# Optimization experiments

Measured on AMD Instinct MI355X. Metric: run time of the kernel, lower is better.

Reference implementation:

```python
import jax, jax.numpy as jnp
import numpy as np
import math

def setup_inputs() -> dict:
    key = jax.random.key(0)
    k1, k2, k3 = jax.random.split(key, 3)
    B, S, E = 2, 2048, 1024
    H, D = 16, 64
    inputs = jax.random.normal(k1, (B, S, E), dtype=jnp.float32)
    Wqkv = jax.random.uniform(k2, (E, 3 * H * D), minval=-0.1, maxval=0.1, dtype=jnp.float32)
    Wo = jax.random.uniform(k3, (H * D, E), minval=-0.1, maxval=0.1, dtype=jnp.float32)
    return {"inputs": inputs, "Wqkv": Wqkv, "Wo": Wo, "nhead": H}

def reference(inputs, Wqkv, Wo, nhead):
    B, S, E = inputs.shape
    H = int(nhead)
    D = Wqkv.shape[1] // (3 * H)
    causal, ghost = True, True

    qkv = jnp.matmul(inputs, Wqkv)                       # (B, S, 3*H*D)
    qkv = qkv.reshape(B, S, 3, H, D)
    Q = qkv[:, :, 0].transpose(0, 2, 1, 3)               # (B, H, S, D)
    K = qkv[:, :, 1].transpose(0, 2, 1, 3)
    V = qkv[:, :, 2].transpose(0, 2, 1, 3)

    scores = jnp.einsum('bhqd,bhkd->bhqk', Q, K) / math.sqrt(D)
    if causal:
        neg_inf = jnp.float32(-jnp.inf)
        mask = jnp.where(jnp.triu(jnp.ones((S, S), dtype=bool), k=1), neg_inf, jnp.float32(0.0))
        scores = scores + mask  # broadcast over (B, H)

    # ghost softmax: standard stable softmax but denominator gets +1
    z = jnp.exp(scores - jnp.max(scores, axis=-1, keepdims=True))
    denom = jnp.sum(z, axis=-1, keepdims=True)
    if ghost:
        denom = denom + jnp.float32(1.0)
    attn = z / denom                                      # (B, H, S, S)

    A = jnp.einsum('bhqk,bhkd->bhqd', attn, V)            # (B, H, S, D)
    A = A.transpose(0, 2, 1, 3).reshape(B, S, H * D)      # (B, S, H*D)
    return jnp.matmul(A, Wo)
```

## Files before the change

### kernel.cpp

```cpp
#include <hip/hip_runtime.h>

typedef float    f32x4  __attribute__((ext_vector_type(4)));
typedef _Float16 half8  __attribute__((ext_vector_type(8)));
typedef _Float16 half4v __attribute__((ext_vector_type(4)));

#define MFMA16(a,b,c) __builtin_amdgcn_mfma_f32_16x16x32_f16(a,b,c,0,0,0)

__device__ __forceinline__ float exp2_fast(float x){
  float y; asm("v_exp_f32 %0, %1" : "=v"(y) : "v"(x)); return y;
}
__device__ __forceinline__ void gload_lds16(const _Float16* g, _Float16* l){
  __builtin_amdgcn_global_load_lds(
      (const __attribute__((address_space(1))) unsigned int*)(g),
      (__attribute__((address_space(3))) unsigned int*)(l),
      16, 0, 0);
}

#define S_LEN 2048
#define E_DIM 1024
#define H_NUM 16
#define D_DIM 64
#define NBH   32
#define M_ROWS 4096
#define N3    3072
#define LOG2E 1.44269504089f

__global__ __launch_bounds__(256) void prep_kernel(
    const float* __restrict__ X, const float* __restrict__ Wqkv,
    const float* __restrict__ Wo,
    _Float16* __restrict__ Xh, _Float16* __restrict__ Wqh,
    _Float16* __restrict__ Woh)
{
  __shared__ float tile[32][33];
  const int blk = blockIdx.x, tid = threadIdx.x;
  if (blk < 4096){
    const int i = blk * 256 + tid;
    const float4 v = reinterpret_cast<const float4*>(X)[i];
    half4v h;
    h[0] = (_Float16)v.x; h[1] = (_Float16)v.y;
    h[2] = (_Float16)v.z; h[3] = (_Float16)v.w;
    *reinterpret_cast<half4v*>(&Xh[(size_t)i*4]) = h;
    return;
  }
  const float* in; _Float16* out; int R, C, bx, by;
  if (blk < 4096 + 3072){
    const int b2 = blk - 4096;
    in = Wqkv; out = Wqh; R = E_DIM; C = N3;
    bx = (b2 % 96) * 32; by = (b2 / 96) * 32;
  } else {
    const int b2 = blk - 7168;
    in = Wo; out = Woh; R = E_DIM; C = E_DIM;
    bx = (b2 % 32) * 32; by = (b2 / 32) * 32;
  }
  const int tx = tid & 31, ty = tid >> 5;
#pragma unroll
  for (int i = ty; i < 32; i += 8)
    tile[i][tx] = in[(size_t)(by + i) * C + bx + tx];
  __syncthreads();
#pragma unroll
  for (int i = ty; i < 32; i += 8)
    out[(size_t)(bx + i) * R + by + tx] = (_Float16)tile[tx][i];
}

template<int EPI>
__global__ __launch_bounds__(256, 3) void gemm97(
    const _Float16* __restrict__ A, const _Float16* __restrict__ B,
    int Kdim, int Ndim, float* __restrict__ Cout,
    _Float16* __restrict__ qh, _Float16* __restrict__ kh, _Float16* __restrict__ vh)
{
  __shared__ __align__(16) _Float16 sA[128][64], sB[128][64];
  const int tid = threadIdx.x;
  const int m0 = blockIdx.y * 128, n0 = blockIdx.x * 128;
  const int wid = tid >> 6, lane = tid & 63;
  const int wr = (wid >> 1) * 64, wc = (wid & 1) * 64;
  const int lr = lane & 15, lc = lane >> 4;
  const int ldrow = lane >> 3;
  const int ldcol = ((lane & 7) ^ ldrow) * 8;
  const int swz = (lr & 7) << 4;

  f32x4 acc[4][4] = {};
  const int nK = Kdim >> 6;
  for (int ks = 0; ks < nK; ++ks){
    const int k0 = ks << 6;
#pragma unroll
    for (int cc = 0; cc < 4; ++cc){
      const int c = wid * 4 + cc;
      const int row = c * 8 + ldrow;
      gload_lds16(&A[(size_t)(m0 + row) * Kdim + k0 + ldcol], &sA[c*8][0]);
      gload_lds16(&B[(size_t)(n0 + row) * Kdim + k0 + ldcol], &sB[c*8][0]);
    }
    __syncthreads();
    const char* ab = (const char*)&sA[0][0];
    const char* bb = (const char*)&sB[0][0];
#pragma unroll
    for (int kk = 0; kk < 64; kk += 32){
      half8 fa[4], fb[4];
#pragma unroll
      for (int t = 0; t < 4; ++t){
        fa[t] = *reinterpret_cast<const half8*>(
            ab + (wr + t*16 + lr)*128 + ((kk*2 + lc*16) ^ swz));
        fb[t] = *reinterpret_cast<const half8*>(
            bb + (wc + t*16 + lr)*128 + ((kk*2 + lc*16) ^ swz));
      }
#pragma unroll
      for (int mt = 0; mt < 4; ++mt)
#pragma unroll
        for (int nt = 0; nt < 4; ++nt)
          acc[mt][nt] = MFMA16(fa[mt], fb[nt], acc[mt][nt]);
    }
    __syncthreads();
  }
#pragma unroll
  for (int mt = 0; mt < 4; ++mt)
#pragma unroll
    for (int nt = 0; nt < 4; ++nt)
#pragma unroll
      for (int r = 0; r < 4; ++r){
        const int m = m0 + wr + mt*16 + lc*4 + r;
        const int n = n0 + wc + nt*16 + lr;
        float v = acc[mt][nt][r];
        if (EPI == 0){
          Cout[(size_t)m * Ndim + n] = v;
        } else {
          const int t = n >> 10, rem = n & 1023, hh = rem >> 6, d = rem & 63;
          const int b = m >> 11, s = m & 2047;
          const int bh = b * H_NUM + hh;
          if (t == 0) v *= (0.125f * LOG2E);
          size_t o;
          if (t == 2)  o = ((size_t)bh * D_DIM + d) * S_LEN + s;
          else         o = ((size_t)bh * S_LEN + s) * D_DIM + d;
          _Float16* ph = (t == 0) ? qh : (t == 1) ? kh : vh;
          ph[o] = (_Float16)v;
        }
      }
}

__global__ __launch_bounds__(256, 4) void gemm64(
    const _Float16* __restrict__ A, const _Float16* __restrict__ B,
    int Kdim, int Ndim, float* __restrict__ Cout)
{
  __shared__ __align__(16) _Float16 sA[64][64], sB[128][64];
  const int tid = threadIdx.x;
  const int m0 = blockIdx.y * 64, n0 = blockIdx.x * 128;
  const int wid = tid >> 6, lane = tid & 63;
  const int wr = (wid >> 1) * 32, wc = (wid & 1) * 64;
  const int lr = lane & 15, lc = lane >> 4;
  const int ldrow = lane >> 3;
  const int ldcol = ((lane & 7) ^ ldrow) * 8;
  const int swz = (lr & 7) << 4;

  f32x4 acc[2][4] = {};
  const int nK = Kdim >> 6;
  for (int ks = 0; ks < nK; ++ks){
    const int k0 = ks << 6;
#pragma unroll
    for (int cc = 0; cc < 2; ++cc){
      const int c = wid * 2 + cc;
      const int row = c * 8 + ldrow;
      gload_lds16(&A[(size_t)(m0 + row) * Kdim + k0 + ldcol], &sA[c*8][0]);
    }
#pragma unroll
    for (int cc = 0; cc < 4; ++cc){
      const int c = wid * 4 + cc;
      const int row = c * 8 + ldrow;
      gload_lds16(&B[(size_t)(n0 + row) * Kdim + k0 + ldcol], &sB[c*8][0]);
    }
    __syncthreads();
    const char* ab = (const char*)&sA[0][0];
    const char* bb = (const char*)&sB[0][0];
#pragma unroll
    for (int kk = 0; kk < 64; kk += 32){
      half8 fa[2], fb[4];
#pragma unroll
      for (int t = 0; t < 2; ++t)
        fa[t] = *reinterpret_cast<const half8*>(
            ab + (wr + t*16 + lr)*128 + ((kk*2 + lc*16) ^ swz));
#pragma unroll
      for (int t = 0; t < 4; ++t)
        fb[t] = *reinterpret_cast<const half8*>(
            bb + (wc + t*16 + lr)*128 + ((kk*2 + lc*16) ^ swz));
#pragma unroll
      for (int mt = 0; mt < 2; ++mt)
#pragma unroll
        for (int nt = 0; nt < 4; ++nt)
          acc[mt][nt] = MFMA16(fa[mt], fb[nt], acc[mt][nt]);
    }
    __syncthreads();
  }
#pragma unroll
  for (int mt = 0; mt < 2; ++mt)
#pragma unroll
    for (int nt = 0; nt < 4; ++nt)
#pragma unroll
      for (int r = 0; r < 4; ++r){
        const int m = m0 + wr + mt*16 + lc*4 + r;
        const int n = n0 + wc + nt*16 + lr;
        Cout[(size_t)m * Ndim + n] = acc[mt][nt][r];
      }
}

__global__ __launch_bounds__(256, 6) void attn_partial(
    const _Float16* __restrict__ Qh, const _Float16* __restrict__ Kh,
    const _Float16* __restrict__ Vth,
    _Float16* __restrict__ Opart, float* __restrict__ Spart)
{
  __shared__ __align__(16) _Float16 sK[64][64];
  __shared__ __align__(16) _Float16 sV[64][64];
  __shared__ __align__(16) _Float16 sP[4][16][64];
  const int tid = threadIdx.x, wid = tid >> 6, lane = tid & 63;
  const int id  = blockIdx.x;
  const int xcd = id & 7, seq = id >> 3;
  const int bh  = xcd + 8 * (seq & 3);
  const int rest = seq >> 2;
  const int qt  = 31 - (rest >> 1);
  const int half = rest & 1;
  const int h0 = (qt + 1) >> 1;
  const int t0 = half ? h0 : 0;
  const int t1 = half ? (qt + 1) : h0;
  const int q0 = qt * 64;
  const int lr = lane & 15, lc = lane >> 4;
  const int swz = (lr & 7) << 4;
  const size_t base = (size_t)bh * S_LEN * D_DIM;

  const int pidx = (bh * 32 + qt) * 2 + half;
  _Float16* Op = Opart + (size_t)pidx * 4096;
  float*    Sp = Spart + (size_t)pidx * 192;

  if (t1 <= t0){
#pragma unroll
    for (int dt = 0; dt < 4; ++dt)
#pragma unroll
      for (int r = 0; r < 4; ++r)
        Op[(wid*16 + lc*4 + r)*64 + dt*16 + lr] = (_Float16)0.f;
    if (lane < 16){
      Sp[wid*16 + lr] = -1e30f;
      Sp[64 + wid*16 + lr] = 0.f;
      Sp[128 + wid*16 + lr] = -1e30f;
    }
    return;
  }

  const int lrow = lane >> 3;
  const int cswz = ((lane & 7) ^ lrow) * 8;

  auto stage = [&](int t){
    const int kv0 = t * 64;
#pragma unroll
    for (int cc = 0; cc < 2; ++cc){
      const int c = wid * 2 + cc;
      const int row = c * 8 + lrow;
      gload_lds16(&Kh[base + (size_t)(kv0 + row) * D_DIM + cswz], &sK[c*8][0]);
      gload_lds16(&Vth[base + (size_t)row * S_LEN + kv0 + cswz], &sV[c*8][0]);
    }
  };

  half8 fq[2];
  {
    const int qrow = q0 + wid*16 + lr;
#pragma unroll
    for (int kc = 0; kc < 2; ++kc)
      fq[kc] = *reinterpret_cast<const half8*>(&Qh[base + (size_t)qrow * 64 + kc*32 + lc*8]);
  }

  f32x4 acc[4] = {};
  float m = -1e30f, l = 0.f, tm = -1e30f;

#pragma unroll 1
  for (int t = t0; t < t1; ++t){
    __syncthreads();
    stage(t);
    __syncthreads();

    const char* kb = (const char*)&sK[0][0];
    f32x4 sc[4];
    __builtin_amdgcn_s_setprio(1);
#pragma unroll
    for (int nt = 0; nt < 4; ++nt){
      f32x4 z = {};
#pragma unroll
      for (int kc = 0; kc < 2; ++kc){
        const half8 fk = *reinterpret_cast<const half8*>(
            kb + (nt*16 + lr)*128 + ((kc*64 + lc*16) ^ swz));
        z = MFMA16(fk, fq[kc], z);
      }
      sc[nt] = z;
    }
    __builtin_amdgcn_s_setprio(0);

    if (t == qt){
#pragma unroll
      for (int nt = 0; nt < 4; ++nt)
#pragma unroll
        for (int r = 0; r < 4; ++r)
          if (nt*16 + lc*4 + r > wid*16 + lr) sc[nt][r] = -1e30f;
    }

    f32x4 a;
#pragma unroll
    for (int j = 0; j < 4; ++j)
      a[j] = fmaxf(fmaxf(sc[0][j], sc[1][j]), fmaxf(sc[2][j], sc[3][j]));
    float mx = fmaxf(fmaxf(a[0], a[1]), fmaxf(a[2], a[3]));
    mx = fmaxf(mx, __shfl_xor(mx, 16));
    mx = fmaxf(mx, __shfl_xor(mx, 32));
    tm = fmaxf(tm, mx);

    if (__any(mx > m + 8.0f)){
      const float mn = fmaxf(m, mx);
      const float s = exp2_fast(m - mn);
      l *= s; m = mn;
      float rs[4];
#pragma unroll
      for (int r = 0; r < 4; ++r)
        rs[r] = __shfl(s, (lc << 4) | (lc*4 + r), 64);
#pragma unroll
      for (int dt = 0; dt < 4; ++dt)
#pragma unroll
        for (int r = 0; r < 4; ++r) acc[dt][r] *= rs[r];
    }

    f32x4 ssum = {};
#pragma unroll
    for (int nt = 0; nt < 4; ++nt){
#pragma unroll
      for (int r = 0; r < 4; ++r) sc[nt][r] = exp2_fast(sc[nt][r] - m);
      ssum += sc[nt];
    }
    float s1 = (ssum[0] + ssum[1]) + (ssum[2] + ssum[3]);
    s1 += __shfl_xor(s1, 16);
    s1 += __shfl_xor(s1, 32);
    l += s1;

    char* pw = (char*)&sP[wid][0][0];
#pragma unroll
    for (int nt = 0; nt < 4; ++nt){
      int2 pk;
      pk.x = __builtin_bit_cast(int, __builtin_amdgcn_cvt_pkrtz(sc[nt][0], sc[nt][1]));
      pk.y = __builtin_bit_cast(int, __builtin_amdgcn_cvt_pkrtz(sc[nt][2], sc[nt][3]));
      *reinterpret_cast<int2*>(pw + lr*128 + ((nt*32 + lc*8) ^ swz)) = pk;
    }

    const half8 pa0 = *reinterpret_cast<const half8*>(pw + lr*128 + ((lc*16) ^ swz));
    const half8 pa1 = *reinterpret_cast<const half8*>(pw + lr*128 + ((64 + lc*16) ^ swz));

    const char* vb = (const char*)&sV[0][0];
    __builtin_amdgcn_s_setprio(1);
#pragma unroll
    for (int dt = 0; dt < 4; ++dt){
#pragma unroll
      for (int kc = 0; kc < 2; ++kc){
        const half8 fv = *reinterpret_cast<const half8*>(
            vb + (dt*16 + lr)*128 + ((kc*64 + lc*16) ^ swz));
        acc[dt] = MFMA16(kc ? pa1 : pa0, fv, acc[dt]);
      }
    }
    __builtin_amdgcn_s_setprio(0);
  }

#pragma unroll
  for (int dt = 0; dt < 4; ++dt)
#pragma unroll
    for (int r = 0; r < 4; ++r)
      Op[(wid*16 + lc*4 + r)*64 + dt*16 + lr] = (_Float16)acc[dt][r];
  if (lane < 16){
    Sp[wid*16 + lr] = m;
    Sp[64 + wid*16 + lr] = l;
    Sp[128 + wid*16 + lr] = tm;
  }
}

__global__ __launch_bounds__(256) void attn_merge(
    const _Float16* __restrict__ Opart, const float* __restrict__ Spart,
    _Float16* __restrict__ Ao)
{
  const int id = blockIdx.x;
  const int bh = id >> 5, qt = id & 31;
  const int tid = threadIdx.x;
  const int row = tid >> 2, seg = tid & 3;
  const int p0 = (bh * 32 + qt) * 2, p1 = p0 + 1;
  const float* S1 = Spart + (size_t)p0 * 192;
  const float* S2 = Spart + (size_t)p1 * 192;
  const float m1 = S1[row], l1 = S1[64 + row], t1 = S1[128 + row];
  const float m2 = S2[row], l2 = S2[64 + row], t2 = S2[128 + row];
  const float M  = fmaxf(m1, m2);
  const float w1 = exp2_fast(m1 - M), w2 = exp2_fast(m2 - M);
  const float den = l1 * w1 + l2 * w2 + exp2_fast(fmaxf(t1, t2) - M);
  const float inv = 1.0f / den;
  const half8* O1 = reinterpret_cast<const half8*>(Opart + (size_t)p0 * 4096 + row * 64 + seg * 16);
  const half8* O2 = reinterpret_cast<const half8*>(Opart + (size_t)p1 * 4096 + row * 64 + seg * 16);
  const int b = bh >> 4, hh = bh & 15;
  const int q = qt * 64 + row;
  _Float16* dst = Ao + ((size_t)(b * S_LEN + q)) * E_DIM + hh * D_DIM + seg * 16;
#pragma unroll
  for (int v = 0; v < 2; ++v){
    const half8 a1 = O1[v], a2 = O2[v];
    half8 o;
#pragma unroll
    for (int j = 0; j < 8; ++j)
      o[j] = (_Float16)(((float)a1[j] * w1 + (float)a2[j] * w2) * inv);
    reinterpret_cast<half8*>(dst)[v] = o;
  }
}

extern "C" void kernel_launch(void* const* d_in, const int* in_sizes, int n_in,
                              void* d_out, int out_size, void* d_ws, size_t ws_size,
                              hipStream_t stream){
  const float* X    = (const float*)d_in[0];
  const float* Wqkv = (const float*)d_in[1];
  const float* Wo   = (const float*)d_in[2];
  float* out = (float*)d_out;

  _Float16* w = (_Float16*)d_ws;
  size_t off = 0;
  auto alloc = [&](size_t n){ _Float16* p = w + off; off += n; return p; };
  const size_t ME   = (size_t)M_ROWS * E_DIM;
  const size_t WQ   = (size_t)N3 * E_DIM;
  const size_t WOsz = (size_t)E_DIM * E_DIM;
  const size_t QK   = (size_t)NBH * S_LEN * D_DIM;
  _Float16 *Xh = alloc(ME);
  _Float16 *Wqh = alloc(WQ);
  _Float16 *Woh = alloc(WOsz);
  _Float16 *Qh = alloc(QK), *Kh = alloc(QK), *Vth = alloc(QK);
  _Float16 *Ahalf = alloc(ME);
  _Float16 *Opart = alloc((size_t)2048 * 4096);
  _Float16 *Sraw  = alloc((size_t)2048 * 192 * 2);
  float* Spart = (float*)Sraw;

  prep_kernel<<<dim3(8192), 256, 0, stream>>>(X, Wqkv, Wo, Xh, Wqh, Woh);

  gemm97<1><<<dim3(N3/128, M_ROWS/128), 256, 0, stream>>>(
      Xh, Wqh, E_DIM, N3, nullptr, Qh, Kh, Vth);

  attn_partial<<<dim3(2048), 256, 0, stream>>>(Qh, Kh, Vth, Opart, Spart);
  attn_merge<<<dim3(1024), 256, 0, stream>>>(Opart, Spart, Ahalf);

  gemm64<<<dim3(E_DIM/128, M_ROWS/64), 256, 0, stream>>>(
      Ahalf, Woh, E_DIM, E_DIM, out);
}
```

Measured before the change: 112.7 us.

## Split KV only for long causal query tiles, finalize short tiles in-kernel

Before, every causal query tile was split into two KV halves, with partials written out and then combined by a merge kernel. Now only the 16 longest query tiles per head are split. The 16 shorter ones run their full KV range in one block, normalize with the ghost-softmax denominator and write directly to the attention output. This drops the partial-buffer traffic, half of the merge work and the empty-split blocks, at the cost of less even block durations across the grid.

```diff
diff --git a/kernel.cpp b/kernel.cpp
--- a/kernel.cpp
+++ b/kernel.cpp
@@ -202,44 +202,35 @@
 __global__ __launch_bounds__(256, 6) void attn_partial(
     const _Float16* __restrict__ Qh, const _Float16* __restrict__ Kh,
     const _Float16* __restrict__ Vth,
-    _Float16* __restrict__ Opart, float* __restrict__ Spart)
+    _Float16* __restrict__ Opart, float* __restrict__ Spart,
+    _Float16* __restrict__ Ao)
 {
   __shared__ __align__(16) _Float16 sK[64][64];
   __shared__ __align__(16) _Float16 sV[64][64];
   __shared__ __align__(16) _Float16 sP[4][16][64];
   const int tid = threadIdx.x, wid = tid >> 6, lane = tid & 63;
   const int id  = blockIdx.x;
-  const int xcd = id & 7, seq = id >> 3;
-  const int bh  = xcd + 8 * (seq & 3);
-  const int rest = seq >> 2;
-  const int qt  = 31 - (rest >> 1);
-  const int half = rest & 1;
-  const int h0 = (qt + 1) >> 1;
-  const int t0 = half ? h0 : 0;
-  const int t1 = half ? (qt + 1) : h0;
+  const int xcd = id & 7;
+  const int bh  = xcd + 8 * ((id >> 3) & 3);
+  const int c   = id >> 5;
+  int qt, t0, t1, split;
+  if (c < 32){
+    qt = 31 - (c >> 1);
+    const int half = c & 1;
+    const int h0 = (qt + 1) >> 1;
+    t0 = half ? h0 : 0;
+    t1 = half ? (qt + 1) : h0;
+    split = 1;
+  } else {
+    qt = 47 - c;
+    t0 = 0; t1 = qt + 1;
+    split = 0;
+  }
   const int q0 = qt * 64;
   const int lr = lane & 15, lc = lane >> 4;
   const int swz = (lr & 7) << 4;
   const size_t base = (size_t)bh * S_LEN * D_DIM;
 
-  const int pidx = (bh * 32 + qt) * 2 + half;
-  _Float16* Op = Opart + (size_t)pidx * 4096;
-  float*    Sp = Spart + (size_t)pidx * 192;
-
-  if (t1 <= t0){
-#pragma unroll
-    for (int dt = 0; dt < 4; ++dt)
-#pragma unroll
-      for (int r = 0; r < 4; ++r)
-        Op[(wid*16 + lc*4 + r)*64 + dt*16 + lr] = (_Float16)0.f;
-    if (lane < 16){
-      Sp[wid*16 + lr] = -1e30f;
-      Sp[64 + wid*16 + lr] = 0.f;
-      Sp[128 + wid*16 + lr] = -1e30f;
-    }
-    return;
-  }
-
   const int lrow = lane >> 3;
   const int cswz = ((lane & 7) ^ lrow) * 8;
 
@@ -247,10 +238,10 @@
     const int kv0 = t * 64;
 #pragma unroll
     for (int cc = 0; cc < 2; ++cc){
-      const int c = wid * 2 + cc;
-      const int row = c * 8 + lrow;
-      gload_lds16(&Kh[base + (size_t)(kv0 + row) * D_DIM + cswz], &sK[c*8][0]);
-      gload_lds16(&Vth[base + (size_t)row * S_LEN + kv0 + cswz], &sV[c*8][0]);
+      const int ch = wid * 2 + cc;
+      const int row = ch * 8 + lrow;
+      gload_lds16(&Kh[base + (size_t)(kv0 + row) * D_DIM + cswz], &sK[ch*8][0]);
+      gload_lds16(&Vth[base + (size_t)row * S_LEN + kv0 + cswz], &sV[ch*8][0]);
     }
   };
 
@@ -356,15 +347,36 @@
     __builtin_amdgcn_s_setprio(0);
   }
 
-#pragma unroll
-  for (int dt = 0; dt < 4; ++dt)
+  if (split){
+    const int pidx = (bh * 16 + (qt - 16)) * 2 + (t0 != 0);
+    _Float16* Op = Opart + (size_t)pidx * 4096;
+    float*    Sp = Spart + (size_t)pidx * 192;
+#pragma unroll
+    for (int dt = 0; dt < 4; ++dt)
+#pragma unroll
+      for (int r = 0; r < 4; ++r)
+        Op[(wid*16 + lc*4 + r)*64 + dt*16 + lr] = (_Float16)acc[dt][r];
+    if (lane < 16){
+      Sp[wid*16 + lr] = m;
+      Sp[64 + wid*16 + lr] = l;
+      Sp[128 + wid*16 + lr] = tm;
+    }
+  } else {
+    const int b = bh >> 4, hh = bh & 15;
+    const float den = l + exp2_fast(tm - m);
+    float rden[4];
 #pragma unroll
     for (int r = 0; r < 4; ++r)
-      Op[(wid*16 + lc*4 + r)*64 + dt*16 + lr] = (_Float16)acc[dt][r];
-  if (lane < 16){
-    Sp[wid*16 + lr] = m;
-    Sp[64 + wid*16 + lr] = l;
-    Sp[128 + wid*16 + lr] = tm;
+      rden[r] = __shfl(den, (lc << 4) | (lc*4 + r), 64);
+#pragma unroll
+    for (int dt = 0; dt < 4; ++dt)
+#pragma unroll
+      for (int r = 0; r < 4; ++r){
+        const float o = acc[dt][r] / rden[r];
+        const int q = q0 + wid*16 + lc*4 + r;
+        const int d = dt*16 + lr;
+        Ao[((size_t)(b*S_LEN + q)) * E_DIM + hh*D_DIM + d] = (_Float16)o;
+      }
   }
 }
 
@@ -373,10 +385,11 @@
     _Float16* __restrict__ Ao)
 {
   const int id = blockIdx.x;
-  const int bh = id >> 5, qt = id & 31;
+  const int bh = id >> 4, qtl = id & 15;
+  const int qt = 16 + qtl;
   const int tid = threadIdx.x;
   const int row = tid >> 2, seg = tid & 3;
-  const int p0 = (bh * 32 + qt) * 2, p1 = p0 + 1;
+  const int p0 = (bh * 16 + qtl) * 2, p1 = p0 + 1;
   const float* S1 = Spart + (size_t)p0 * 192;
   const float* S2 = Spart + (size_t)p1 * 192;
   const float m1 = S1[row], l1 = S1[64 + row], t1 = S1[128 + row];
@@ -421,8 +434,8 @@
   _Float16 *Woh = alloc(WOsz);
   _Float16 *Qh = alloc(QK), *Kh = alloc(QK), *Vth = alloc(QK);
   _Float16 *Ahalf = alloc(ME);
-  _Float16 *Opart = alloc((size_t)2048 * 4096);
-  _Float16 *Sraw  = alloc((size_t)2048 * 192 * 2);
+  _Float16 *Opart = alloc((size_t)1024 * 4096);
+  _Float16 *Sraw  = alloc((size_t)1024 * 192 * 2);
   float* Spart = (float*)Sraw;
 
   prep_kernel<<<dim3(8192), 256, 0, stream>>>(X, Wqkv, Wo, Xh, Wqh, Woh);
@@ -430,8 +443,8 @@
   gemm97<1><<<dim3(N3/128, M_ROWS/128), 256, 0, stream>>>(
       Xh, Wqh, E_DIM, N3, nullptr, Qh, Kh, Vth);
 
-  attn_partial<<<dim3(2048), 256, 0, stream>>>(Qh, Kh, Vth, Opart, Spart);
-  attn_merge<<<dim3(1024), 256, 0, stream>>>(Opart, Spart, Ahalf);
+  attn_partial<<<dim3(1536), 256, 0, stream>>>(Qh, Kh, Vth, Opart, Spart, Ahalf);
+  attn_merge<<<dim3(512), 256, 0, stream>>>(Opart, Spart, Ahalf);
 
   gemm64<<<dim3(E_DIM/128, M_ROWS/64), 256, 0, stream>>>(
       Ahalf, Woh, E_DIM, E_DIM, out);
```

New measurement: 115.9 us. +2.9%, slower.

## Split causal attention KV range into 1-4 partitions per query tile by length

Applied to the files above, without the earlier changes.

Replaces the fixed two-way KV split per query tile with a variable split: tiles with longer causal ranges get up to four partitions, short ones get one. This removes the empty blocks that short tiles produced and makes block work more uniform across the grid (2560 blocks instead of 2048). The merge kernel now combines a variable number of partials, and the partial buffers are enlarged to hold four per tile. The cost is more partial writes and reads in the merge step and a slightly more complex index mapping.

```diff
diff --git a/kernel.cpp b/kernel.cpp
--- a/kernel.cpp
+++ b/kernel.cpp
@@ -209,37 +209,21 @@
   __shared__ __align__(16) _Float16 sP[4][16][64];
   const int tid = threadIdx.x, wid = tid >> 6, lane = tid & 63;
   const int id  = blockIdx.x;
-  const int xcd = id & 7, seq = id >> 3;
-  const int bh  = xcd + 8 * (seq & 3);
-  const int rest = seq >> 2;
-  const int qt  = 31 - (rest >> 1);
-  const int half = rest & 1;
-  const int h0 = (qt + 1) >> 1;
-  const int t0 = half ? h0 : 0;
-  const int t1 = half ? (qt + 1) : h0;
+  const int xcd = id & 7;
+  const int bh  = xcd + 8 * ((id >> 3) & 3);
+  const int k   = id >> 5;
+  int qt, np, p;
+  if (k < 32)      { qt = 31 - (k >> 2);        np = 4; p = k & 3; }
+  else if (k < 56) { const int j = k - 32; qt = 23 - j / 3; np = 3; p = j % 3; }
+  else if (k < 72) { const int j = k - 56; qt = 15 - (j >> 1); np = 2; p = j & 1; }
+  else             { qt = 7 - (k - 72);         np = 1; p = 0; }
+  const int t0 = p * (qt + 1) / np;
+  const int t1 = (p + 1) * (qt + 1) / np;
   const int q0 = qt * 64;
   const int lr = lane & 15, lc = lane >> 4;
   const int swz = (lr & 7) << 4;
   const size_t base = (size_t)bh * S_LEN * D_DIM;
 
-  const int pidx = (bh * 32 + qt) * 2 + half;
-  _Float16* Op = Opart + (size_t)pidx * 4096;
-  float*    Sp = Spart + (size_t)pidx * 192;
-
-  if (t1 <= t0){
-#pragma unroll
-    for (int dt = 0; dt < 4; ++dt)
-#pragma unroll
-      for (int r = 0; r < 4; ++r)
-        Op[(wid*16 + lc*4 + r)*64 + dt*16 + lr] = (_Float16)0.f;
-    if (lane < 16){
-      Sp[wid*16 + lr] = -1e30f;
-      Sp[64 + wid*16 + lr] = 0.f;
-      Sp[128 + wid*16 + lr] = -1e30f;
-    }
-    return;
-  }
-
   const int lrow = lane >> 3;
   const int cswz = ((lane & 7) ^ lrow) * 8;
 
@@ -247,10 +231,10 @@
     const int kv0 = t * 64;
 #pragma unroll
     for (int cc = 0; cc < 2; ++cc){
-      const int c = wid * 2 + cc;
-      const int row = c * 8 + lrow;
-      gload_lds16(&Kh[base + (size_t)(kv0 + row) * D_DIM + cswz], &sK[c*8][0]);
-      gload_lds16(&Vth[base + (size_t)row * S_LEN + kv0 + cswz], &sV[c*8][0]);
+      const int ch = wid * 2 + cc;
+      const int row = ch * 8 + lrow;
+      gload_lds16(&Kh[base + (size_t)(kv0 + row) * D_DIM + cswz], &sK[ch*8][0]);
+      gload_lds16(&Vth[base + (size_t)row * S_LEN + kv0 + cswz], &sV[ch*8][0]);
     }
   };
 
@@ -356,6 +340,9 @@
     __builtin_amdgcn_s_setprio(0);
   }
 
+  const int pidx = (bh * 32 + qt) * 4 + p;
+  _Float16* Op = Opart + (size_t)pidx * 4096;
+  float*    Sp = Spart + (size_t)pidx * 192;
 #pragma unroll
   for (int dt = 0; dt < 4; ++dt)
 #pragma unroll
@@ -374,30 +361,42 @@
 {
   const int id = blockIdx.x;
   const int bh = id >> 5, qt = id & 31;
+  const int np = (qt >> 3) + 1;
   const int tid = threadIdx.x;
   const int row = tid >> 2, seg = tid & 3;
-  const int p0 = (bh * 32 + qt) * 2, p1 = p0 + 1;
-  const float* S1 = Spart + (size_t)p0 * 192;
-  const float* S2 = Spart + (size_t)p1 * 192;
-  const float m1 = S1[row], l1 = S1[64 + row], t1 = S1[128 + row];
-  const float m2 = S2[row], l2 = S2[64 + row], t2 = S2[128 + row];
-  const float M  = fmaxf(m1, m2);
-  const float w1 = exp2_fast(m1 - M), w2 = exp2_fast(m2 - M);
-  const float den = l1 * w1 + l2 * w2 + exp2_fast(fmaxf(t1, t2) - M);
+  const int pbase = (bh * 32 + qt) * 4;
+
+  float mi[4], li[4], ti[4];
+  float M = -1e30f, T = -1e30f;
+  for (int i = 0; i < np; ++i){
+    const float* Sp = Spart + (size_t)(pbase + i) * 192;
+    mi[i] = Sp[row]; li[i] = Sp[64 + row]; ti[i] = Sp[128 + row];
+    M = fmaxf(M, mi[i]); T = fmaxf(T, ti[i]);
+  }
+  float den = exp2_fast(T - M);
+  float wgt[4];
+  for (int i = 0; i < np; ++i){
+    wgt[i] = exp2_fast(mi[i] - M);
+    den += li[i] * wgt[i];
+  }
   const float inv = 1.0f / den;
-  const half8* O1 = reinterpret_cast<const half8*>(Opart + (size_t)p0 * 4096 + row * 64 + seg * 16);
-  const half8* O2 = reinterpret_cast<const half8*>(Opart + (size_t)p1 * 4096 + row * 64 + seg * 16);
+
   const int b = bh >> 4, hh = bh & 15;
   const int q = qt * 64 + row;
   _Float16* dst = Ao + ((size_t)(b * S_LEN + q)) * E_DIM + hh * D_DIM + seg * 16;
 #pragma unroll
   for (int v = 0; v < 2; ++v){
-    const half8 a1 = O1[v], a2 = O2[v];
-    half8 o;
-#pragma unroll
-    for (int j = 0; j < 8; ++j)
-      o[j] = (_Float16)(((float)a1[j] * w1 + (float)a2[j] * w2) * inv);
-    reinterpret_cast<half8*>(dst)[v] = o;
+    float o[8] = {};
+    for (int i = 0; i < np; ++i){
+      const half8 ai = reinterpret_cast<const half8*>(
+          Opart + (size_t)(pbase + i) * 4096 + row * 64 + seg * 16)[v];
+#pragma unroll
+      for (int j = 0; j < 8; ++j) o[j] += (float)ai[j] * wgt[i];
+    }
+    half8 h;
+#pragma unroll
+    for (int j = 0; j < 8; ++j) h[j] = (_Float16)(o[j] * inv);
+    reinterpret_cast<half8*>(dst)[v] = h;
   }
 }
 
@@ -421,8 +420,8 @@
   _Float16 *Woh = alloc(WOsz);
   _Float16 *Qh = alloc(QK), *Kh = alloc(QK), *Vth = alloc(QK);
   _Float16 *Ahalf = alloc(ME);
-  _Float16 *Opart = alloc((size_t)2048 * 4096);
-  _Float16 *Sraw  = alloc((size_t)2048 * 192 * 2);
+  _Float16 *Opart = alloc((size_t)4096 * 4096);
+  _Float16 *Sraw  = alloc((size_t)4096 * 192 * 2);
   float* Spart = (float*)Sraw;
 
   prep_kernel<<<dim3(8192), 256, 0, stream>>>(X, Wqkv, Wo, Xh, Wqh, Woh);
@@ -430,7 +429,7 @@
   gemm97<1><<<dim3(N3/128, M_ROWS/128), 256, 0, stream>>>(
       Xh, Wqh, E_DIM, N3, nullptr, Qh, Kh, Vth);
 
-  attn_partial<<<dim3(2048), 256, 0, stream>>>(Qh, Kh, Vth, Opart, Spart);
+  attn_partial<<<dim3(2560), 256, 0, stream>>>(Qh, Kh, Vth, Opart, Spart);
   attn_merge<<<dim3(1024), 256, 0, stream>>>(Opart, Spart, Ahalf);
 
   gemm64<<<dim3(E_DIM/128, M_ROWS/64), 256, 0, stream>>>(
```

After: 117.8 us. +4.6%, slower.
